# Performance work log

Measured on AMD Instinct MI355X. Metric: run time of the kernel, lower is better.

Reference implementation:

```python
import jax, jax.numpy as jnp
import numpy as np

WINDOW_SIZE = 512  # init kwarg

def setup_inputs() -> dict:
    key = jax.random.key(0)
    kq, kk, kv = jax.random.split(key, 3)
    B, H, S, D = 1, 16, 4096, 64
    q = jax.random.normal(kq, (B, H, S, D), dtype=jnp.float32)
    k = jax.random.normal(kk, (B, H, S, D), dtype=jnp.float32)
    v = jax.random.normal(kv, (B, H, S, D), dtype=jnp.float32)
    return {"q": q, "k": k, "v": v}

def reference(q, k, v):
    # q,k,v: [B, H, S, D]
    B, H, S, D = q.shape
    scale = 1.0 / jnp.sqrt(jnp.asarray(D, dtype=q.dtype))
    scores = jnp.einsum('bhqd,bhkd->bhqk', q, k) * scale  # [B,H,S,S]
    # sliding-window band mask: token i attends to j in [i - w//2, i + w//2]
    idx = jnp.arange(S)
    band = jnp.abs(idx[:, None] - idx[None, :]) <= (WINDOW_SIZE // 2)  # [S,S]
    scores = jnp.where(band, scores, -jnp.inf)  # same as adding -inf mask
    probs = jax.nn.softmax(scores, axis=-1)
    return jnp.einsum('bhqk,bhkd->bhqd', probs, v)
```

## Files before the change

### kernel.cpp

```cpp
#include <hip/hip_runtime.h>
#include <math.h>

#define SEQ   4096
#define HD    64
#define NH    16
#define WHALF 256
#define QB    128
#define KT    128
#define KSTR  72
#define VSTR  136
#define KPLANE (KT * KSTR)
#define VPLANE (HD * VSTR)
#define BUFSZ  (KPLANE + VPLANE)

typedef __attribute__((ext_vector_type(8))) __bf16 bf16x8;
typedef __attribute__((ext_vector_type(8))) short short8v;
typedef __attribute__((ext_vector_type(4))) float f32x4;

__device__ __forceinline__ short bf16bits(float x) {
    __bf16 b = (__bf16)x;
    return __builtin_bit_cast(short, b);
}

#define MFMA32(A, B, C) __builtin_amdgcn_mfma_f32_16x16x32_bf16((A), (B), (C), 0, 0, 0)

#if __has_builtin(__builtin_amdgcn_exp2f)
#define EXP2F(x) __builtin_amdgcn_exp2f(x)
#else
#define EXP2F(x) __exp2f(x)
#endif

__global__ __launch_bounds__(512, 4)
void swa_mfma10_kernel(const float* __restrict__ q,
                       const float* __restrict__ k,
                       const float* __restrict__ v,
                       float* __restrict__ out) {
    __shared__ short smem[2 * BUFSZ];

    const int orig = blockIdx.x;
    const int work = ((orig & 7) << 6) + (orig >> 3);
    const int h    = work >> 5;
    const int q0   = (work & 31) * QB;

    const int t    = threadIdx.x;
    const int lane = t & 63;
    const int w    = t >> 6;
    const int n15  = lane & 15;
    const int g    = lane >> 4;
    const int qrow = q0 + w * 16 + n15;

    const float SCALE = 0.125f * 1.44269504088896340736f;

    bf16x8 qf[2];
    {
        const float* qp = q + ((size_t)h * SEQ + qrow) * HD;
        #pragma unroll
        for (int c = 0; c < 2; ++c) {
            const float4* p4 = reinterpret_cast<const float4*>(qp + 32 * c + 8 * g);
            float4 a = p4[0], b = p4[1];
            float xs[8] = {a.x, a.y, a.z, a.w, b.x, b.y, b.z, b.w};
            short8v q8;
            #pragma unroll
            for (int j = 0; j < 8; ++j) q8[j] = bf16bits(xs[j] * SCALE);
            qf[c] = __builtin_bit_cast(bf16x8, q8);
        }
    }

    bf16x8 ones8;
    {
        short8v o8;
        const short ov = (n15 == 0) ? (short)0x3F80 : (short)0;
        #pragma unroll
        for (int j = 0; j < 8; ++j) o8[j] = ov;
        ones8 = __builtin_bit_cast(bf16x8, o8);
    }

    f32x4 accO[4];
    #pragma unroll
    for (int dt = 0; dt < 4; ++dt) accO[dt] = (f32x4){0.f, 0.f, 0.f, 0.f};
    f32x4 accL = (f32x4){0.f, 0.f, 0.f, 0.f};

    int k0 = q0 - WHALF;           if (k0 < 0) k0 = 0;
    int k1 = q0 + QB - 1 + WHALF;  if (k1 > SEQ - 1) k1 = SEQ - 1;
    const int nt = (k1 + 1 - k0) >> 7;

    const int wqmin = q0 + w * 16;
    const int wqmax = wqmin + 15;
    const int wlo   = wqmin - WHALF;
    const int whi   = wqmax + WHALF;

    const float4* kb4 = reinterpret_cast<const float4*>(k + ((size_t)h * SEQ) * HD);
    const float*  vp  = v + ((size_t)h * SEQ) * HD;

    float4 kreg[4];
    float  vreg[16];

    #define LOADT(KTV)                                                        \
        {                                                                     \
            const int kt_ = (KTV);                                            \
            _Pragma("unroll")                                                 \
            for (int i = 0; i < 4; ++i)                                       \
                kreg[i] = kb4[(size_t)kt_ * 16 + t * 4 + i];                  \
            _Pragma("unroll")                                                 \
            for (int j = 0; j < 16; ++j)                                      \
                vreg[j] = vp[(size_t)(kt_ + 16 * w + j) * HD + lane];         \
        }

    auto STAGE = [&](int b) {
        short* Kb = smem + b * BUFSZ;
        short* Vb = Kb + KPLANE;

        const int p  = t >> 2;
        const int q5 = p & 31;
        const int R  = (p & 96) + (((q5 >> 2) & 1) << 4) + ((q5 >> 3) << 2) + (q5 & 3);

        const float* kf = reinterpret_cast<const float*>(&kreg[0]);
        short8v k8a, k8b;
        #pragma unroll
        for (int j = 0; j < 8; ++j) {
            k8a[j] = bf16bits(kf[j]);
            k8b[j] = bf16bits(kf[8 + j]);
        }
        *reinterpret_cast<short8v*>(&Kb[R * KSTR + (t & 3) * 16])     = k8a;
        *reinterpret_cast<short8v*>(&Kb[R * KSTR + (t & 3) * 16 + 8]) = k8b;

        short8v v8a, v8b;
        #pragma unroll
        for (int j = 0; j < 8; ++j) {
            v8a[j] = bf16bits(vreg[j]);
            v8b[j] = bf16bits(vreg[8 + j]);
        }
        *reinterpret_cast<short8v*>(&Vb[lane * VSTR + 16 * w])     = v8a;
        *reinterpret_cast<short8v*>(&Vb[lane * VSTR + 16 * w + 8]) = v8b;
    };

    LOADT(k0);
    STAGE(0);
    if (nt > 1) LOADT(k0 + KT);
    __syncthreads();

    for (int i = 0; i < nt; ++i) {
        const int kt  = k0 + i * KT;
        const int cur = i & 1;

        if (i + 1 < nt) {
            STAGE(cur ^ 1);
            if (i + 2 < nt) LOADT(k0 + (i + 2) * KT);
        }

        const short* Kb = smem + cur * BUFSZ;
        const short* Vb = Kb + KPLANE;

        #pragma unroll
        for (int kc = 0; kc < 4; ++kc) {
            const int cb = kt + kc * 32;
            if (cb > whi || cb + 31 < wlo) continue;

            f32x4 S[2];
            __builtin_amdgcn_s_setprio(1);
            #pragma unroll
            for (int s = 0; s < 2; ++s) {
                const int krow = (kc * 32 + s * 16 + n15) * KSTR + 8 * g;
                bf16x8 k0f = __builtin_bit_cast(bf16x8, *reinterpret_cast<const short8v*>(&Kb[krow]));
                bf16x8 k1f = __builtin_bit_cast(bf16x8, *reinterpret_cast<const short8v*>(&Kb[krow + 32]));
                f32x4 a = (f32x4){0.f, 0.f, 0.f, 0.f};
                a = MFMA32(k0f, qf[0], a);
                a = MFMA32(k1f, qf[1], a);
                S[s] = a;
            }
            __builtin_amdgcn_s_setprio(0);

            short8v p8s;
            const bool interior = (cb >= wqmax - WHALF) && (cb + 31 <= wqmin + WHALF);
            if (interior) {
                #pragma unroll
                for (int j = 0; j < 8; ++j)
                    p8s[j] = bf16bits(EXP2F(S[j >> 2][j & 3]));
            } else {
                const int kbase = cb + 8 * g;
                #pragma unroll
                for (int j = 0; j < 8; ++j) {
                    int key = kbase + j;
                    bool valid = (key >= qrow - WHALF) && (key <= qrow + WHALF);
                    p8s[j] = bf16bits(EXP2F(valid ? S[j >> 2][j & 3] : -1e30f));
                }
            }
            bf16x8 p8 = __builtin_bit_cast(bf16x8, p8s);

            __builtin_amdgcn_s_setprio(1);
            #pragma unroll
            for (int dt = 0; dt < 4; ++dt) {
                const int vrow = (dt * 16 + n15) * VSTR + kc * 32 + 8 * g;
                bf16x8 vf = __builtin_bit_cast(bf16x8, *reinterpret_cast<const short8v*>(&Vb[vrow]));
                accO[dt] = MFMA32(vf, p8, accO[dt]);
            }
            accL = MFMA32(ones8, p8, accL);
            __builtin_amdgcn_s_setprio(0);
        }

        if (i + 1 < nt) __syncthreads();
    }

    const float lsum = __shfl(accL[0], n15);
    const float inv  = 1.0f / lsum;
    float* op = out + ((size_t)h * SEQ + qrow) * HD;
    #pragma unroll
    for (int dt = 0; dt < 4; ++dt) {
        *reinterpret_cast<f32x4*>(op + dt * 16 + 4 * g) = accO[dt] * inv;
    }
}

extern "C" void kernel_launch(void* const* d_in, const int* in_sizes, int n_in,
                              void* d_out, int out_size, void* d_ws, size_t ws_size,
                              hipStream_t stream) {
    const float* q = (const float*)d_in[0];
    const float* k = (const float*)d_in[1];
    const float* v = (const float*)d_in[2];
    float* out = (float*)d_out;

    dim3 grid(NH * (SEQ / QB));
    dim3 block(512);
    hipLaunchKernelGGL(swa_mfma10_kernel, grid, block, 0, stream, q, k, v, out);
}
```

Measured before the change: 27.34 us.

## Double-buffer K/V prefetch registers and use an LDS-only barrier

Splits the K/V prefetch registers into two alternating sets. The next tile's global loads are now issued before the current registers are converted and written to shared memory, so loads run further ahead of compute. It also replaces __syncthreads with a barrier that waits only on LDS counters, so in-flight global loads stay outstanding across the barrier instead of being drained. In exchange, register pressure roughly doubles for the prefetch buffers under a 512-thread, 4-block launch bound, which risks spills or lower occupancy. The final iterations also reload a redundant tile.

```diff
diff --git a/kernel.cpp b/kernel.cpp
--- a/kernel.cpp
+++ b/kernel.cpp
@@ -30,8 +30,10 @@
 #define EXP2F(x) __exp2f(x)
 #endif
 
+#define TILE_BARRIER() asm volatile("s_waitcnt lgkmcnt(0)\n\ts_barrier" ::: "memory")
+
 __global__ __launch_bounds__(512, 4)
-void swa_mfma10_kernel(const float* __restrict__ q,
+void swa_mfma11_kernel(const float* __restrict__ q,
                        const float* __restrict__ k,
                        const float* __restrict__ v,
                        float* __restrict__ out) {
@@ -92,21 +94,19 @@
     const float4* kb4 = reinterpret_cast<const float4*>(k + ((size_t)h * SEQ) * HD);
     const float*  vp  = v + ((size_t)h * SEQ) * HD;
 
-    float4 kreg[4];
-    float  vreg[16];
-
-    #define LOADT(KTV)                                                        \
-        {                                                                     \
-            const int kt_ = (KTV);                                            \
-            _Pragma("unroll")                                                 \
-            for (int i = 0; i < 4; ++i)                                       \
-                kreg[i] = kb4[(size_t)kt_ * 16 + t * 4 + i];                  \
-            _Pragma("unroll")                                                 \
-            for (int j = 0; j < 16; ++j)                                      \
-                vreg[j] = vp[(size_t)(kt_ + 16 * w + j) * HD + lane];         \
-        }
-
-    auto STAGE = [&](int b) {
+    float4 kregA[4], kregB[4];
+    float  vregA[16], vregB[16];
+
+    auto LOADT = [&](float4 (&kr)[4], float (&vr)[16], int kt_) {
+        #pragma unroll
+        for (int i2 = 0; i2 < 4; ++i2)
+            kr[i2] = kb4[(size_t)kt_ * 16 + t * 4 + i2];
+        #pragma unroll
+        for (int j = 0; j < 16; ++j)
+            vr[j] = vp[(size_t)(kt_ + 16 * w + j) * HD + lane];
+    };
+
+    auto STAGE = [&](int b, const float4 (&kr)[4], const float (&vr)[16]) {
         short* Kb = smem + b * BUFSZ;
         short* Vb = Kb + KPLANE;
 
@@ -114,7 +114,7 @@
         const int q5 = p & 31;
         const int R  = (p & 96) + (((q5 >> 2) & 1) << 4) + ((q5 >> 3) << 2) + (q5 & 3);
 
-        const float* kf = reinterpret_cast<const float*>(&kreg[0]);
+        const float* kf = reinterpret_cast<const float*>(&kr[0]);
         short8v k8a, k8b;
         #pragma unroll
         for (int j = 0; j < 8; ++j) {
@@ -127,25 +127,26 @@
         short8v v8a, v8b;
         #pragma unroll
         for (int j = 0; j < 8; ++j) {
-            v8a[j] = bf16bits(vreg[j]);
-            v8b[j] = bf16bits(vreg[8 + j]);
+            v8a[j] = bf16bits(vr[j]);
+            v8b[j] = bf16bits(vr[8 + j]);
         }
         *reinterpret_cast<short8v*>(&Vb[lane * VSTR + 16 * w])     = v8a;
         *reinterpret_cast<short8v*>(&Vb[lane * VSTR + 16 * w + 8]) = v8b;
     };
 
-    LOADT(k0);
-    STAGE(0);
-    if (nt > 1) LOADT(k0 + KT);
-    __syncthreads();
+    LOADT(kregA, vregA, k0);
+    STAGE(0, kregA, vregA);
+    if (nt > 1) LOADT(kregB, vregB, k0 + KT);
+    TILE_BARRIER();
 
     for (int i = 0; i < nt; ++i) {
         const int kt  = k0 + i * KT;
         const int cur = i & 1;
 
         if (i + 1 < nt) {
-            STAGE(cur ^ 1);
-            if (i + 2 < nt) LOADT(k0 + (i + 2) * KT);
+            const int ktn = k0 + ((i + 2 < nt) ? (i + 2) : (nt - 1)) * KT;
+            if (cur) { LOADT(kregB, vregB, ktn); STAGE(cur ^ 1, kregA, vregA); }
+            else     { LOADT(kregA, vregA, ktn); STAGE(cur ^ 1, kregB, vregB); }
         }
 
         const short* Kb = smem + cur * BUFSZ;
@@ -198,7 +199,7 @@
             __builtin_amdgcn_s_setprio(0);
         }
 
-        if (i + 1 < nt) __syncthreads();
+        if (i + 1 < nt) TILE_BARRIER();
     }
 
     const float lsum = __shfl(accL[0], n15);
@@ -220,5 +221,5 @@
 
     dim3 grid(NH * (SEQ / QB));
     dim3 block(512);
-    hipLaunchKernelGGL(swa_mfma10_kernel, grid, block, 0, stream, q, k, v, out);
+    hipLaunchKernelGGL(swa_mfma11_kernel, grid, block, 0, stream, q, k, v, out);
 }
```

After: 74.40 us. +172.1%, slower.
